# Kernel tuning notes

Hardware: AMD Instinct MI355X
Metric: run time of the kernel (lower is better)

Reference implementation:

```python
import jax, jax.numpy as jnp
import numpy as np

B, S, D, H, E, K = 4, 2048, 1024, 2048, 8, 2


def setup_inputs() -> dict:
    key = jax.random.key(0)
    ks = jax.random.split(key, 5)
    x = jax.random.normal(ks[0], (B, S, D), dtype=jnp.float32)
    Wr = jax.random.normal(ks[1], (D, E), dtype=jnp.float32) * 0.02  # router weight
    w1 = jax.random.normal(ks[2], (E, D, H), dtype=jnp.float32) * 0.02  # gate proj per expert
    w3 = jax.random.normal(ks[3], (E, D, H), dtype=jnp.float32) * 0.02  # up proj per expert
    w2 = jax.random.normal(ks[4], (E, H, D), dtype=jnp.float32) * 0.02  # down proj per expert
    return {"x": x, "Wr": Wr, "w1": w1, "w2": w2, "w3": w3}


def reference(x, Wr, w1, w2, w3):
    b, s, d = x.shape
    e = Wr.shape[1]
    flat = x.reshape(b * s, d)                      # [T, D]
    logits = flat @ Wr                              # [T, E]
    probs = jax.nn.softmax(logits, axis=-1)
    vals, idx = jax.lax.top_k(probs, K)             # [T, K]
    weights = vals / jnp.sum(vals, axis=-1, keepdims=True)
    onehot = jax.nn.one_hot(idx, e, dtype=flat.dtype)   # [T, K, E]
    cw = jnp.einsum('tke,tk->te', onehot, weights)      # combine weight per (token, expert)

    # naive dense: every expert computes every token, masked by combine weights
    out = jnp.zeros_like(flat)
    for ei in range(e):  # fixed small structural loop over experts
        h = jax.nn.silu(flat @ w1[ei]) * (flat @ w3[ei])   # [T, H]
        out = out + (h @ w2[ei]) * cw[:, ei:ei + 1]

    # aux load-balancing loss (usage uses any() over top-k slots, as in torch code)
    usage = (onehot.sum(axis=1) > 0).astype(flat.dtype).mean(axis=0)  # [E]
    prob_mass = probs.mean(axis=0)                                     # [E]
    aux_loss = e * jnp.sum(usage * prob_mass)
    return out.reshape(b, s, d), aux_loss
```

## Files before the change

kernel.cpp:

```cpp
#include <hip/hip_runtime.h>
#include <hip/hip_bf16.h>
#include <cstdint>
#include <cstddef>

#define T_TOK 8192
#define DIM   1024
#define HID   2048
#define NE    8
#define CAP   2816

typedef __attribute__((ext_vector_type(8))) short bf16x8;
typedef __attribute__((ext_vector_type(4))) float f32x4;
using bf16 = __hip_bfloat16;

__device__ __forceinline__ void gload16(const bf16* g, bf16* l) {
    __builtin_amdgcn_global_load_lds(
        (const __attribute__((address_space(1))) unsigned int*)(g),
        (__attribute__((address_space(3))) unsigned int*)(l), 16, 0, 0);
}
__device__ __forceinline__ float b2f(unsigned short u) {
    return __uint_as_float(((unsigned int)u) << 16);
}
#define MFMA16(a, b, c) __builtin_amdgcn_mfma_f32_16x16x32_bf16((a), (b), (c), 0, 0, 0)

__global__ __launch_bounds__(256) void k_transpose_all(const float* __restrict__ w1,
                                                       const float* __restrict__ w3,
                                                       const float* __restrict__ w2,
                                                       bf16* __restrict__ w1t,
                                                       bf16* __restrict__ w3t,
                                                       bf16* __restrict__ w2t) {
    __shared__ float tile[64][65];
    int z = blockIdx.z;
    const float* in = (z == 0) ? w1 : (z == 1) ? w3 : w2;
    bf16* out = (z == 0) ? w1t : (z == 1) ? w3t : w2t;
    int R = (z == 2) ? HID : DIM;
    int C = (z == 2) ? DIM : HID;
    int e = blockIdx.y;
    int ct = C >> 6;
    int r0 = (blockIdx.x / ct) << 6;
    int c0 = (blockIdx.x % ct) << 6;
    const float* src = in + (size_t)e * R * C;
    bf16* dst = out + (size_t)e * R * C;
    int s = threadIdx.x & 15, g = threadIdx.x >> 4;
#pragma unroll
    for (int j = 0; j < 4; ++j) {
        int row = j * 16 + g;
        float4 v = *(const float4*)(src + (size_t)(r0 + row) * C + c0 + s * 4);
        tile[row][s * 4 + 0] = v.x; tile[row][s * 4 + 1] = v.y;
        tile[row][s * 4 + 2] = v.z; tile[row][s * 4 + 3] = v.w;
    }
    __syncthreads();
#pragma unroll
    for (int j = 0; j < 4; ++j) {
        int c = j * 16 + g;
        int r = s * 4;
        bf16 o[4] = {__float2bfloat16(tile[r][c]),     __float2bfloat16(tile[r + 1][c]),
                     __float2bfloat16(tile[r + 2][c]), __float2bfloat16(tile[r + 3][c])};
        *(uint2*)(dst + (size_t)(c0 + c) * R + r0 + r) = *(const uint2*)o;
    }
}

__global__ __launch_bounds__(256) void k_logits(const float* __restrict__ x,
                                                const float* __restrict__ Wr,
                                                float* __restrict__ logits,
                                                bf16* __restrict__ xb) {
    __shared__ float wl[NE][DIM];
    for (int o = threadIdx.x; o < NE * DIM; o += 256) {
        int e = o >> 10, d = o & (DIM - 1);
        wl[e][d] = Wr[d * NE + e];
    }
    __syncthreads();
    int wid = threadIdx.x >> 6, lane = threadIdx.x & 63;
    int t = blockIdx.x * 4 + wid;
    const float* xr = x + (size_t)t * DIM;
    double acc[NE];
#pragma unroll
    for (int e = 0; e < NE; ++e) acc[e] = 0.0;
#pragma unroll
    for (int i = 0; i < DIM / 256; ++i) {
        int base = i * 256 + lane * 4;
        float4 v = *(const float4*)(xr + base);
        bf16 o[4] = {__float2bfloat16(v.x), __float2bfloat16(v.y),
                     __float2bfloat16(v.z), __float2bfloat16(v.w)};
        *(uint2*)(xb + (size_t)t * DIM + base) = *(const uint2*)o;
#pragma unroll
        for (int e = 0; e < NE; ++e)
            acc[e] += (double)v.x * wl[e][base] + (double)v.y * wl[e][base + 1]
                    + (double)v.z * wl[e][base + 2] + (double)v.w * wl[e][base + 3];
    }
#pragma unroll
    for (int e = 0; e < NE; ++e) {
        double v = acc[e];
        for (int m = 32; m >= 1; m >>= 1) v += __shfl_xor(v, m);
        if (lane == 0) logits[t * NE + e] = (float)v;
    }
}

__global__ __launch_bounds__(256) void k_route(const float* __restrict__ logits,
                                               int* counts, int* seg_tok, float* seg_w,
                                               int* slotpos, float* probsum) {
    int t = blockIdx.x * 256 + threadIdx.x;
    float l[NE];
#pragma unroll
    for (int e = 0; e < NE; ++e) l[e] = logits[t * NE + e];
    float mx = l[0];
#pragma unroll
    for (int e = 1; e < NE; ++e) mx = fmaxf(mx, l[e]);
    float p[NE], s = 0.f;
#pragma unroll
    for (int e = 0; e < NE; ++e) { p[e] = expf(l[e] - mx); s += p[e]; }
    float inv = 1.f / s;
#pragma unroll
    for (int e = 0; e < NE; ++e) p[e] *= inv;
    int e0 = 0; float v0 = p[0];
#pragma unroll
    for (int e = 1; e < NE; ++e) if (p[e] > v0) { v0 = p[e]; e0 = e; }
    int e1 = -1; float v1 = -1.f;
#pragma unroll
    for (int e = 0; e < NE; ++e) if (e != e0 && p[e] > v1) { v1 = p[e]; e1 = e; }
    float wsum = v0 + v1;
    float w0 = v0 / wsum, w1 = v1 / wsum;

    int lane = threadIdx.x & 63, wid = threadIdx.x >> 6;
    __shared__ float ps[4][NE];
#pragma unroll
    for (int e = 0; e < NE; ++e) {
        float v = p[e];
        for (int m = 32; m >= 1; m >>= 1) v += __shfl_xor(v, m);
        if (lane == 0) ps[wid][e] = v;
    }
    __syncthreads();
    if (threadIdx.x < NE) {
        float v = ps[0][threadIdx.x] + ps[1][threadIdx.x] + ps[2][threadIdx.x] + ps[3][threadIdx.x];
        atomicAdd(&probsum[threadIdx.x], v);
    }
    for (int slot = 0; slot < 2; ++slot) {
        int   e  = slot ? e1 : e0;
        float wv = slot ? w1 : w0;
#pragma unroll
        for (int ex = 0; ex < NE; ++ex) {
            unsigned long long m = __ballot(e == ex);
            if (e == ex) {
                int leader = __ffsll(m) - 1;
                int base = 0;
                if (lane == leader) base = atomicAdd(&counts[ex], __popcll(m));
                base = __shfl(base, leader);
                int pos = base + (int)__popcll(m & ((1ull << lane) - 1ull));
                if (pos < CAP) {
                    seg_tok[ex * CAP + pos] = t;
                    seg_w[ex * CAP + pos]  = wv;
                    slotpos[2 * t + slot]  = ex * CAP + pos;
                } else {
                    slotpos[2 * t + slot]  = -1;
                }
            }
        }
    }
}

__global__ __launch_bounds__(512, 2) void k_gemm1(const bf16* __restrict__ xb,
                                                  const bf16* __restrict__ w1t,
                                                  const bf16* __restrict__ w3t,
                                                  const int* __restrict__ counts,
                                                  const int* __restrict__ seg_tok,
                                                  bf16* __restrict__ h) {
    __shared__ __align__(16) bf16 lds[24576];
    __shared__ int toks[128];
    const int NTL = HID / 128;
    int flat = blockIdx.y * gridDim.x + blockIdx.x;
    int cpx  = (gridDim.x * NE) >> 3;
    int swz  = (flat & 7) * cpx + (flat >> 3);
    int e    = swz / gridDim.x;
    int tile = swz % gridDim.x;
    int mtile = tile / NTL, ntile = tile % NTL;
    int cnt = counts[e]; if (cnt > CAP) cnt = CAP;
    if (mtile * 128 >= cnt) return;

    int tx = threadIdx.x, lane = tx & 63, w = tx >> 6;
    if (tx < 128) {
        int slot = mtile * 128 + tx;
        toks[tx] = seg_tok[e * CAP + (slot < cnt ? slot : 0)];
    }
    __syncthreads();

    int l8 = lane >> 3;
    int sch = (((lane & 7) ^ l8) << 3);
    const bf16* sp[6];
    bf16* dp[6];
#pragma unroll
    for (int i = 0; i < 6; ++i) {
        int c = w * 6 + i;
        dp[i] = lds + c * 512 + (lane << 3);
        if (c < 16)
            sp[i] = xb + (size_t)toks[c * 8 + l8] * DIM + sch;
        else if (c < 32)
            sp[i] = w1t + ((size_t)e * HID + ntile * 128 + (c - 16) * 8 + l8) * DIM + sch;
        else
            sp[i] = w3t + ((size_t)e * HID + ntile * 128 + (c - 32) * 8 + l8) * DIM + sch;
    }

    int l15 = lane & 15, lh = lane >> 4;
    int role = w >> 2, rh = (w >> 1) & 1, ch = w & 1;
    const int bbase = 8192 + role * 8192;
    f32x4 acc[4][4];
    f32x4 zero4 = {0.f, 0.f, 0.f, 0.f};
#pragma unroll
    for (int m = 0; m < 4; ++m)
#pragma unroll
        for (int n = 0; n < 4; ++n) acc[m][n] = zero4;

    const int NT = DIM / 64;
#pragma unroll 1
    for (int k = 0; k < NT; ++k) {
        int ko = k * 64;
#pragma unroll
        for (int i = 0; i < 6; ++i) gload16(sp[i] + ko, dp[i]);
        __syncthreads();
#pragma unroll
        for (int ks = 0; ks < 2; ++ks) {
            int co = ((((ks << 2) | lh) ^ (l15 & 7)) << 3);
            bf16x8 af[4], bb[4];
#pragma unroll
            for (int m = 0; m < 4; ++m)
                af[m] = *(const bf16x8*)(lds + (rh * 64 + m * 16 + l15) * 64 + co);
#pragma unroll
            for (int n = 0; n < 4; ++n)
                bb[n] = *(const bf16x8*)(lds + bbase + (ch * 64 + n * 16 + l15) * 64 + co);
#pragma unroll
            for (int n = 0; n < 4; ++n)
#pragma unroll
                for (int m = 0; m < 4; ++m)
                    acc[m][n] = MFMA16(af[m], bb[n], acc[m][n]);
        }
        __syncthreads();
    }

    if (role == 1) {
#pragma unroll
        for (int m = 0; m < 4; ++m)
#pragma unroll
            for (int n = 0; n < 4; ++n)
#pragma unroll
                for (int r = 0; r < 4; ++r) {
                    int row = rh * 64 + m * 16 + lh * 4 + r;
                    int col = ch * 64 + n * 16 + l15;
                    lds[row * 128 + col] = __float2bfloat16(acc[m][n][r]);
                }
    }
    __syncthreads();
    if (role == 0) {
        bf16* hdst = h + ((size_t)e * CAP + (size_t)mtile * 128) * HID + ntile * 128;
#pragma unroll
        for (int m = 0; m < 4; ++m)
#pragma unroll
            for (int n = 0; n < 4; ++n)
#pragma unroll
                for (int r = 0; r < 4; ++r) {
                    int row = rh * 64 + m * 16 + lh * 4 + r;
                    int col = ch * 64 + n * 16 + l15;
                    float gg = acc[m][n][r];
                    float uu = b2f(*(const unsigned short*)&lds[row * 128 + col]);
                    float hv = gg / (1.f + __expf(-gg)) * uu;
                    hdst[(size_t)row * HID + col] = __float2bfloat16(hv);
                }
    }
}

__global__ __launch_bounds__(512, 2) void k_gemm2(const bf16* __restrict__ hbuf,
                                                  const bf16* __restrict__ w2t,
                                                  const int* __restrict__ counts,
                                                  const float* __restrict__ seg_w,
                                                  bf16* __restrict__ ybuf) {
    __shared__ __align__(16) bf16 lds[24576];
    __shared__ float wts[128];
    const int NTL = DIM / 256;
    int flat = blockIdx.y * gridDim.x + blockIdx.x;
    int cpx  = (gridDim.x * NE) >> 3;
    int swz  = (flat & 7) * cpx + (flat >> 3);
    int e    = swz / gridDim.x;
    int tile = swz % gridDim.x;
    int mtile = tile / NTL, ntile = tile % NTL;
    int cnt = counts[e]; if (cnt > CAP) cnt = CAP;
    if (mtile * 128 >= cnt) return;

    int tx = threadIdx.x, lane = tx & 63, w = tx >> 6;
    if (tx < 128) {
        int slot = mtile * 128 + tx;
        wts[tx] = (slot < cnt) ? seg_w[e * CAP + slot] : 0.f;
    }
    __syncthreads();

    int l8 = lane >> 3;
    int sch = (((lane & 7) ^ l8) << 3);
    const bf16* sp[6];
    bf16* dp[6];
#pragma unroll
    for (int i = 0; i < 6; ++i) {
        int c = w * 6 + i;
        dp[i] = lds + c * 512 + (lane << 3);
        if (c < 16)
            sp[i] = hbuf + ((size_t)e * CAP + mtile * 128 + c * 8 + l8) * HID + sch;
        else
            sp[i] = w2t + ((size_t)e * DIM + ntile * 256 + (c - 16) * 8 + l8) * HID + sch;
    }

    int l15 = lane & 15, lh = lane >> 4;
    int wm = w >> 2, wn = w & 3;
    f32x4 acc[4][4];
    f32x4 zero4 = {0.f, 0.f, 0.f, 0.f};
#pragma unroll
    for (int m = 0; m < 4; ++m)
#pragma unroll
        for (int n = 0; n < 4; ++n) acc[m][n] = zero4;

    const int NT = HID / 64;
#pragma unroll 1
    for (int k = 0; k < NT; ++k) {
        int ko = k * 64;
#pragma unroll
        for (int i = 0; i < 6; ++i) gload16(sp[i] + ko, dp[i]);
        __syncthreads();
#pragma unroll
        for (int ks = 0; ks < 2; ++ks) {
            int co = ((((ks << 2) | lh) ^ (l15 & 7)) << 3);
            bf16x8 af[4], bb[4];
#pragma unroll
            for (int m = 0; m < 4; ++m)
                af[m] = *(const bf16x8*)(lds + (wm * 64 + m * 16 + l15) * 64 + co);
#pragma unroll
            for (int n = 0; n < 4; ++n)
                bb[n] = *(const bf16x8*)(lds + 8192 + (wn * 64 + n * 16 + l15) * 64 + co);
#pragma unroll
            for (int n = 0; n < 4; ++n)
#pragma unroll
                for (int m = 0; m < 4; ++m)
                    acc[m][n] = MFMA16(af[m], bb[n], acc[m][n]);
        }
        __syncthreads();
    }

    bf16* ydst = ybuf + ((size_t)e * CAP + (size_t)mtile * 128) * DIM + ntile * 256;
#pragma unroll
    for (int m = 0; m < 4; ++m)
#pragma unroll
        for (int n = 0; n < 4; ++n)
#pragma unroll
            for (int r = 0; r < 4; ++r) {
                int row = wm * 64 + m * 16 + lh * 4 + r;
                int col = wn * 64 + n * 16 + l15;
                ydst[(size_t)row * DIM + col] = __float2bfloat16(acc[m][n][r] * wts[row]);
            }
}

__global__ __launch_bounds__(256) void k_combine(const bf16* __restrict__ yb,
                                                 const int* __restrict__ slotpos,
                                                 float* __restrict__ out) {
    int t = blockIdx.x;
    int s0 = slotpos[2 * t], s1 = slotpos[2 * t + 1];
    int d = threadIdx.x * 4;
    float4 a = {0.f, 0.f, 0.f, 0.f};
    if (s0 >= 0) {
        ushort4 v = *(const ushort4*)(yb + (size_t)s0 * DIM + d);
        a.x += b2f(v.x); a.y += b2f(v.y); a.z += b2f(v.z); a.w += b2f(v.w);
    }
    if (s1 >= 0) {
        ushort4 v = *(const ushort4*)(yb + (size_t)s1 * DIM + d);
        a.x += b2f(v.x); a.y += b2f(v.y); a.z += b2f(v.z); a.w += b2f(v.w);
    }
    *(float4*)(out + (size_t)t * DIM + d) = a;
}

__global__ void k_aux(const int* __restrict__ counts, const float* __restrict__ probsum,
                      float* __restrict__ outaux) {
    if (threadIdx.x == 0 && blockIdx.x == 0) {
        float s = 0.f;
        for (int e = 0; e < NE; ++e)
            s += ((float)counts[e] / (float)T_TOK) * (probsum[e] / (float)T_TOK);
        *outaux = (float)NE * s;
    }
}

extern "C" void kernel_launch(void* const* d_in, const int* in_sizes, int n_in,
                              void* d_out, int out_size, void* d_ws, size_t ws_size,
                              hipStream_t stream) {
    const float* x  = (const float*)d_in[0];
    const float* Wr = (const float*)d_in[1];
    const float* w1 = (const float*)d_in[2];
    const float* w2 = (const float*)d_in[3];
    const float* w3 = (const float*)d_in[4];
    float* out = (float*)d_out;

    char* ws = (char*)d_ws;
    size_t off = 0;
    auto alloc = [&](size_t bytes) { void* p = ws + off; off += (bytes + 255) & ~(size_t)255; return p; };
    bf16*  xb      = (bf16*)alloc((size_t)T_TOK * DIM * 2);
    bf16*  w1t     = (bf16*)alloc((size_t)NE * HID * DIM * 2);
    bf16*  w3t     = (bf16*)alloc((size_t)NE * HID * DIM * 2);
    bf16*  w2t     = (bf16*)alloc((size_t)NE * DIM * HID * 2);
    bf16*  hbuf    = (bf16*)alloc((size_t)NE * CAP * HID * 2);
    float* logits  = (float*)alloc((size_t)T_TOK * NE * 4);
    int*   counts  = (int*)alloc(256);
    int*   segtok  = (int*)alloc((size_t)NE * CAP * 4);
    float* segw    = (float*)alloc((size_t)NE * CAP * 4);
    int*   slotpos = (int*)alloc((size_t)T_TOK * 2 * 4);
    float* probsum = (float*)alloc(256);
    bf16*  ybuf    = w1t;
    (void)ws_size; (void)in_sizes; (void)n_in;

    hipMemsetAsync(counts, 0, 256, stream);
    hipMemsetAsync(probsum, 0, 256, stream);

    k_logits<<<T_TOK / 4, 256, 0, stream>>>(x, Wr, logits, xb);
    k_route<<<T_TOK / 256, 256, 0, stream>>>(logits, counts, segtok, segw, slotpos, probsum);

    dim3 gt((DIM / 64) * (HID / 64), NE, 3);
    k_transpose_all<<<gt, 256, 0, stream>>>(w1, w3, w2, w1t, w3t, w2t);

    dim3 g1((CAP / 128) * (HID / 128), NE);
    k_gemm1<<<g1, 512, 0, stream>>>(xb, w1t, w3t, counts, segtok, hbuf);
    dim3 g2((CAP / 128) * (DIM / 256), NE);
    k_gemm2<<<g2, 512, 0, stream>>>(hbuf, w2t, counts, segw, ybuf);

    k_combine<<<T_TOK, 256, 0, stream>>>(ybuf, slotpos, out);
    k_aux<<<1, 64, 0, stream>>>(counts, probsum, out + (size_t)T_TOK * DIM);
}
```

Before: 391.3 us.

## Stage GEMM epilogues through LDS, retile down-projection to 128x128, fold aux into combine

The gate/up GEMM epilogue now writes the SiLU-gated hidden tile to LDS and then stores it to global memory with 16-byte vector writes instead of scattered 2-byte stores. The down-projection GEMM is retiled from 128x256 with 512 threads to 128x128 with 256 threads and 3 blocks per SM, and gets the same LDS-staged vectorized epilogue. The separate aux-loss kernel is folded into the combine kernel, which removes one launch. Smaller tiles double the grid and improve occupancy, but each block reuses less data, so more global loads are issued per FLOP.

```diff
diff --git a/kernel.cpp b/kernel.cpp
--- a/kernel.cpp
+++ b/kernel.cpp
@@ -249,7 +249,6 @@
     }
     __syncthreads();
     if (role == 0) {
-        bf16* hdst = h + ((size_t)e * CAP + (size_t)mtile * 128) * HID + ntile * 128;
 #pragma unroll
         for (int m = 0; m < 4; ++m)
 #pragma unroll
@@ -261,19 +260,29 @@
                     float gg = acc[m][n][r];
                     float uu = b2f(*(const unsigned short*)&lds[row * 128 + col]);
                     float hv = gg / (1.f + __expf(-gg)) * uu;
-                    hdst[(size_t)row * HID + col] = __float2bfloat16(hv);
+                    lds[row * 128 + col] = __float2bfloat16(hv);
                 }
     }
-}
-
-__global__ __launch_bounds__(512, 2) void k_gemm2(const bf16* __restrict__ hbuf,
+    __syncthreads();
+    {
+        bf16* hdst = h + ((size_t)e * CAP + (size_t)mtile * 128) * HID + ntile * 128;
+#pragma unroll
+        for (int j = 0; j < 4; ++j) {
+            int idx = tx * 32 + j * 8;
+            int row = idx >> 7, col = idx & 127;
+            *(bf16x8*)(hdst + (size_t)row * HID + col) = *(const bf16x8*)(lds + idx);
+        }
+    }
+}
+
+__global__ __launch_bounds__(256, 3) void k_gemm2(const bf16* __restrict__ hbuf,
                                                   const bf16* __restrict__ w2t,
                                                   const int* __restrict__ counts,
                                                   const float* __restrict__ seg_w,
                                                   bf16* __restrict__ ybuf) {
-    __shared__ __align__(16) bf16 lds[24576];
+    __shared__ __align__(16) bf16 lds[16384];
     __shared__ float wts[128];
-    const int NTL = DIM / 256;
+    const int NTL = DIM / 128;
     int flat = blockIdx.y * gridDim.x + blockIdx.x;
     int cpx  = (gridDim.x * NE) >> 3;
     int swz  = (flat & 7) * cpx + (flat >> 3);
@@ -292,20 +301,18 @@
 
     int l8 = lane >> 3;
     int sch = (((lane & 7) ^ l8) << 3);
-    const bf16* sp[6];
-    bf16* dp[6];
-#pragma unroll
-    for (int i = 0; i < 6; ++i) {
-        int c = w * 6 + i;
-        dp[i] = lds + c * 512 + (lane << 3);
-        if (c < 16)
-            sp[i] = hbuf + ((size_t)e * CAP + mtile * 128 + c * 8 + l8) * HID + sch;
-        else
-            sp[i] = w2t + ((size_t)e * DIM + ntile * 256 + (c - 16) * 8 + l8) * HID + sch;
-    }
+    const bf16* sA[4];
+    const bf16* sB[4];
+#pragma unroll
+    for (int i = 0; i < 4; ++i) {
+        sA[i] = hbuf + ((size_t)e * CAP + mtile * 128 + w * 32 + i * 8 + l8) * HID + sch;
+        sB[i] = w2t + ((size_t)e * DIM + ntile * 128 + w * 32 + i * 8 + l8) * HID + sch;
+    }
+    bf16* dA = lds + w * 2048 + (lane << 3);
+    bf16* dB = lds + 8192 + w * 2048 + (lane << 3);
 
     int l15 = lane & 15, lh = lane >> 4;
-    int wm = w >> 2, wn = w & 3;
+    int wm = w >> 1, wn = w & 1;
     f32x4 acc[4][4];
     f32x4 zero4 = {0.f, 0.f, 0.f, 0.f};
 #pragma unroll
@@ -318,28 +325,31 @@
     for (int k = 0; k < NT; ++k) {
         int ko = k * 64;
 #pragma unroll
-        for (int i = 0; i < 6; ++i) gload16(sp[i] + ko, dp[i]);
+        for (int i = 0; i < 4; ++i) {
+            gload16(sA[i] + ko, dA + i * 512);
+            gload16(sB[i] + ko, dB + i * 512);
+        }
         __syncthreads();
 #pragma unroll
         for (int ks = 0; ks < 2; ++ks) {
             int co = ((((ks << 2) | lh) ^ (l15 & 7)) << 3);
-            bf16x8 af[4], bb[4];
-#pragma unroll
-            for (int m = 0; m < 4; ++m)
-                af[m] = *(const bf16x8*)(lds + (wm * 64 + m * 16 + l15) * 64 + co);
+            bf16x8 af[4], bf_[4];
+#pragma unroll
+            for (int m = 0; m < 4; ++m) {
+                int row = wm * 64 + m * 16 + l15;
+                af[m] = *(const bf16x8*)(lds + row * 64 + co);
+                int br = wn * 64 + m * 16 + l15;
+                bf_[m] = *(const bf16x8*)(lds + 8192 + br * 64 + co);
+            }
 #pragma unroll
             for (int n = 0; n < 4; ++n)
-                bb[n] = *(const bf16x8*)(lds + 8192 + (wn * 64 + n * 16 + l15) * 64 + co);
-#pragma unroll
-            for (int n = 0; n < 4; ++n)
 #pragma unroll
                 for (int m = 0; m < 4; ++m)
-                    acc[m][n] = MFMA16(af[m], bb[n], acc[m][n]);
+                    acc[m][n] = MFMA16(af[m], bf_[n], acc[m][n]);
         }
         __syncthreads();
     }
 
-    bf16* ydst = ybuf + ((size_t)e * CAP + (size_t)mtile * 128) * DIM + ntile * 256;
 #pragma unroll
     for (int m = 0; m < 4; ++m)
 #pragma unroll
@@ -348,12 +358,24 @@
             for (int r = 0; r < 4; ++r) {
                 int row = wm * 64 + m * 16 + lh * 4 + r;
                 int col = wn * 64 + n * 16 + l15;
-                ydst[(size_t)row * DIM + col] = __float2bfloat16(acc[m][n][r] * wts[row]);
+                lds[row * 128 + col] = __float2bfloat16(acc[m][n][r] * wts[row]);
             }
+    __syncthreads();
+    {
+        bf16* ydst = ybuf + ((size_t)e * CAP + (size_t)mtile * 128) * DIM + ntile * 128;
+#pragma unroll
+        for (int j = 0; j < 8; ++j) {
+            int idx = tx * 64 + j * 8;
+            int row = idx >> 7, col = idx & 127;
+            *(bf16x8*)(ydst + (size_t)row * DIM + col) = *(const bf16x8*)(lds + idx);
+        }
+    }
 }
 
 __global__ __launch_bounds__(256) void k_combine(const bf16* __restrict__ yb,
                                                  const int* __restrict__ slotpos,
+                                                 const int* __restrict__ counts,
+                                                 const float* __restrict__ probsum,
                                                  float* __restrict__ out) {
     int t = blockIdx.x;
     int s0 = slotpos[2 * t], s1 = slotpos[2 * t + 1];
@@ -368,15 +390,11 @@
         a.x += b2f(v.x); a.y += b2f(v.y); a.z += b2f(v.z); a.w += b2f(v.w);
     }
     *(float4*)(out + (size_t)t * DIM + d) = a;
-}
-
-__global__ void k_aux(const int* __restrict__ counts, const float* __restrict__ probsum,
-                      float* __restrict__ outaux) {
-    if (threadIdx.x == 0 && blockIdx.x == 0) {
+    if (t == 0 && threadIdx.x == 0) {
         float s = 0.f;
         for (int e = 0; e < NE; ++e)
             s += ((float)counts[e] / (float)T_TOK) * (probsum[e] / (float)T_TOK);
-        *outaux = (float)NE * s;
+        out[(size_t)T_TOK * DIM] = (float)NE * s;
     }
 }
 
@@ -418,9 +436,8 @@
 
     dim3 g1((CAP / 128) * (HID / 128), NE);
     k_gemm1<<<g1, 512, 0, stream>>>(xb, w1t, w3t, counts, segtok, hbuf);
-    dim3 g2((CAP / 128) * (DIM / 256), NE);
-    k_gemm2<<<g2, 512, 0, stream>>>(hbuf, w2t, counts, segw, ybuf);
-
-    k_combine<<<T_TOK, 256, 0, stream>>>(ybuf, slotpos, out);
-    k_aux<<<1, 64, 0, stream>>>(counts, probsum, out + (size_t)T_TOK * DIM);
-}
+    dim3 g2((CAP / 128) * (DIM / 128), NE);
+    k_gemm2<<<g2, 256, 0, stream>>>(hbuf, w2t, counts, segw, ybuf);
+
+    k_combine<<<T_TOK, 256, 0, stream>>>(ybuf, slotpos, counts, probsum, out);
+}
```

Result: slower. 400.6 us (+2.4%).
